# Kernel optimization log

Measured on AMD Instinct MI355X. Metric: run time of the kernel, lower is better.

## Reference

```python
import jax, jax.numpy as jnp
import numpy as np


def quat_to_rot(q):
    # q: [B, 4] = (x, y, z, w); same math as from_quaternion in the source.
    x, y, z, w = q[:, 0], q[:, 1], q[:, 2], q[:, 3]
    tx, ty, tz = 2.0 * x, 2.0 * y, 2.0 * z
    twx, twy, twz = tx * w, ty * w, tz * w
    txx, txy, txz = tx * x, ty * x, tz * x
    tyy, tyz, tzz = ty * y, tz * y, tz * z
    r = jnp.stack([1.0 - (tyy + tzz), txy - twz, txz + twy,
                   txy + twz, 1.0 - (txx + tzz), tyz - twx,
                   txz - twy, tyz + twx, 1.0 - (txx + tyy)], axis=-1)
    return r.reshape(-1, 3, 3)


def matrix_from_params(transfos):
    B, N = transfos.shape
    R = quat_to_rot(transfos[:, :4])
    if N == 10:
        S = jax.vmap(jnp.diag)(transfos[:, -3:])
    else:
        S = jnp.broadcast_to(jnp.eye(3, dtype=transfos.dtype), (B, 3, 3))
    SR = jnp.matmul(S, R)
    if N == 7:
        t = transfos[:, 4:7][..., None]
    else:
        t = jnp.zeros((B, 3, 1), transfos.dtype)
    return jnp.concatenate([SR, t], axis=2)  # [B, 3, 4]


def spatial_transformer_3d(img, transfos, min_ref_grid, max_ref_grid):
    B, H, W, D, C = img.shape  # ref_size_xyz = (W, H, D) per the source
    theta = matrix_from_params(transfos)  # [B, 3, 4]

    xs = jnp.linspace(min_ref_grid[0], max_ref_grid[0], W)
    ys = jnp.linspace(min_ref_grid[1], max_ref_grid[1], H)
    zs = jnp.linspace(min_ref_grid[2], max_ref_grid[2], D)
    mz, my, mx = jnp.meshgrid(zs, ys, xs, indexing='ij')  # (D, H, W), x fastest
    Nel = D * H * W
    grid = jnp.stack([mx.ravel(), my.ravel(), mz.ravel(),
                      jnp.ones(Nel, dtype=img.dtype)], axis=0)  # (4, Nel)
    pts = jnp.einsum('bij,jn->bin', theta, grid)  # (B, 3, Nel)

    Wf, Hf, Df = float(W), float(H), float(D)
    cx = (Wf - 1.0) / (max_ref_grid[0] - min_ref_grid[0])
    cy = (Hf - 1.0) / (max_ref_grid[1] - min_ref_grid[1])
    cz = (Df - 1.0) / (max_ref_grid[2] - min_ref_grid[2])
    ix = cx * pts[:, 0, :] - cx * min_ref_grid[0]
    iy = cy * pts[:, 1, :] - cy * min_ref_grid[1]
    iz = cz * pts[:, 2, :] - cz * min_ref_grid[2]

    # padding_mode in {'zeros','min'}: validity mask for out-of-grid points
    valid = ((ix >= 0.0) & (ix <= Wf - 1.0) &
             (iy >= 0.0) & (iy <= Hf - 1.0) &
             (iz >= 0.0) & (iz <= Df - 1.0)).astype(img.dtype)[..., None]  # (B, Nel, 1)

    ix0 = jnp.clip(jnp.floor(ix), 0.0, Wf - 1.0)
    iy0 = jnp.clip(jnp.floor(iy), 0.0, Hf - 1.0)
    iz0 = jnp.clip(jnp.floor(iz), 0.0, Df - 1.0)

    imf = img.reshape(B, H * W * D, C)
    acc = jnp.zeros((B, Nel, C), img.dtype)
    for ox in (0.0, 1.0):
        for oy in (0.0, 1.0):
            for oz in (0.0, 1.0):
                gx, gy, gz = ix0 + ox, iy0 + oy, iz0 + oz  # corner coords
                w = (jnp.clip(1.0 - jnp.abs(ix - gx), 0.0, 1.0) *
                     jnp.clip(1.0 - jnp.abs(iy - gy), 0.0, 1.0) *
                     jnp.clip(1.0 - jnp.abs(iz - gz), 0.0, 1.0))
                gxi = jnp.clip(gx, 0.0, Wf - 1.0).astype(jnp.int32)
                gyi = jnp.clip(gy, 0.0, Hf - 1.0).astype(jnp.int32)
                gzi = jnp.clip(gz, 0.0, Df - 1.0).astype(jnp.int32)
                lin = (gyi * W + gxi) * D + gzi  # row-major index into [H, W, D]
                v = jnp.take_along_axis(imf, lin[..., None], axis=1)  # (B, Nel, C)
                acc = acc + w[..., None] * v

    # padding_mode == 'min': fill out-of-grid voxels with the per-volume minimum
    fill = jnp.min(img, axis=(1, 2, 3, 4))[:, None, None]  # (B, 1, 1)
    out = valid * acc + (1.0 - valid) * fill
    # grid was flattened in (z, y, x) order with x fastest -> back to (H, W, D)
    out = out.reshape(B, D, H, W, C).transpose(0, 2, 3, 1, 4)
    return out


def setup_inputs() -> dict:
    key = jax.random.key(0)
    k1, k2 = jax.random.split(key)
    img = jax.random.normal(k1, (4, 160, 160, 160, 1), dtype=jnp.float32)
    transfos = jax.random.normal(k2, (4, 7), dtype=jnp.float32)
    return {"img": img, "transfos": transfos}


def reference(img, transfos):
    min_ref_grid = (-1.0, -1.0, -1.0)
    max_ref_grid = (1.0, 1.0, 1.0)
    return spatial_transformer_3d(img, transfos, min_ref_grid, max_ref_grid)
```

## Files before the change

### kernel.cpp

```cpp
#include <hip/hip_runtime.h>

#define HH 160
#define WW 160
#define DD 160
#define BB 4
#define NPB (HH * WW * DD / 4)
#define K1B 256

typedef float vfloat4 __attribute__((ext_vector_type(4)));

__global__ __launch_bounds__(256) void min_cst_kernel(const float4* __restrict__ img4,
                                                      const float* __restrict__ transfos,
                                                      float* __restrict__ partial,
                                                      double* __restrict__ cst) {
    const int b = blockIdx.y;
    const size_t base = (size_t)b * NPB;
    const int t0 = blockIdx.x * 256 + threadIdx.x;
    const int S = K1B * 256;

    float m = 3.4e38f;
    #pragma unroll
    for (int r = 0; r < 4; r++) {
        const int i0 = t0 + 4 * r * S;
        float4 v0 = img4[base + i0];
        float4 v1 = img4[base + i0 + S];
        float4 v2 = img4[base + i0 + 2 * S];
        float4 v3 = make_float4(3.4e38f, 3.4e38f, 3.4e38f, 3.4e38f);
        if (i0 + 3 * S < NPB) v3 = img4[base + i0 + 3 * S];
        m = fminf(m, fminf(fminf(v0.x, v0.y), fminf(v0.z, v0.w)));
        m = fminf(m, fminf(fminf(v1.x, v1.y), fminf(v1.z, v1.w)));
        m = fminf(m, fminf(fminf(v2.x, v2.y), fminf(v2.z, v2.w)));
        m = fminf(m, fminf(fminf(v3.x, v3.y), fminf(v3.z, v3.w)));
    }

    #pragma unroll
    for (int o = 32; o >= 1; o >>= 1) m = fminf(m, __shfl_down(m, o));
    __shared__ float s[4];
    const int lane = threadIdx.x & 63, wid = threadIdx.x >> 6;
    if (lane == 0) s[wid] = m;
    __syncthreads();
    if (threadIdx.x == 0) {
        partial[b * K1B + blockIdx.x] =
            fminf(fminf(s[0], s[1]), fminf(s[2], s[3]));
    }

    if (blockIdx.x == 0 && blockIdx.y == 0 && threadIdx.x < BB) {
        const int bb = threadIdx.x;
        const float* q = transfos + bb * 7;
        double x = q[0], y = q[1], z = q[2], w = q[3];
        double tx = 2.0 * x, ty = 2.0 * y, tz = 2.0 * z;
        double twx = tx * w, twy = ty * w, twz = tz * w;
        double txx = tx * x, txy = ty * x, txz = tz * x;
        double tyy = ty * y, tyz = tz * y, tzz = tz * z;
        double R[3][3] = {
            {1.0 - (tyy + tzz), txy - twz,         txz + twy},
            {txy + twz,         1.0 - (txx + tzz), tyz - twx},
            {txz - twy,         tyz + twx,         1.0 - (txx + tyy)}
        };
        double t[3] = {(double)q[4], (double)q[5], (double)q[6]};
        for (int r = 0; r < 3; r++) {
            cst[bb * 12 + r * 4 + 0] = R[r][0];
            cst[bb * 12 + r * 4 + 1] = R[r][1];
            cst[bb * 12 + r * 4 + 2] = R[r][2];
            cst[bb * 12 + r * 4 + 3] = 79.5 * (t[r] - R[r][0] - R[r][1] - R[r][2] + 1.0);
        }
    }
}

__global__ __launch_bounds__(256) void st3d_kernel(const float* __restrict__ img,
                                                   const double* __restrict__ cst,
                                                   const float* __restrict__ partial,
                                                   float* __restrict__ out) {
    const int bzc = blockIdx.z;
    const int b = bzc / 20;
    const int yt = bzc - b * 20;

    __shared__ float sred[4];
    float pm = partial[b * K1B + threadIdx.x];
    #pragma unroll
    for (int o = 32; o >= 1; o >>= 1) pm = fminf(pm, __shfl_down(pm, o));
    if ((threadIdx.x & 63) == 0) sred[threadIdx.x >> 6] = pm;
    __syncthreads();
    const float fill = fminf(fminf(sred[0], sred[1]), fminf(sred[2], sred[3]));

    const int tz = threadIdx.x & 3;
    const int tx = (threadIdx.x >> 2) & 7;
    const int ty = threadIdx.x >> 5;

    const int x  = blockIdx.y * 8 + tx;
    const int y  = yt * 8 + ty;
    const int zq = blockIdx.x * 16 + tz * 4;

    const double* c = cst + b * 12;
    const double c2 = c[2], c6 = c[6], c10 = c[10];
    const double dx = (double)x, dy = (double)y, dz = (double)zq;
    double ixd = fma(c[0], dx, fma(c[1], dy, fma(c2, dz, c[3])));
    double iyd = fma(c[4], dx, fma(c[5], dy, fma(c6, dz, c[7])));
    double izd = fma(c[8], dx, fma(c[9], dy, fma(c10, dz, c[11])));

    bool anyv = false;
    {
        double ax = ixd, ay = iyd, az = izd;
        #pragma unroll
        for (int k = 0; k < 4; k++) {
            anyv = anyv || ((ax >= 0.0) && (ax <= 159.0) && (ay >= 0.0) &&
                            (ay <= 159.0) && (az >= 0.0) && (az <= 159.0));
            ax += c2; ay += c6; az += c10;
        }
    }

    const float* base = img + (size_t)b * (HH * WW * DD);
    vfloat4 r;

    if (__any(anyv)) {
        #pragma unroll
        for (int k = 0; k < 4; k++) {
            const bool valid = (ixd >= 0.0) && (ixd <= 159.0) && (iyd >= 0.0) &&
                               (iyd <= 159.0) && (izd >= 0.0) && (izd <= 159.0);
            double flx = floor(ixd), fly = floor(iyd), flz = floor(izd);
            int x0 = (int)flx, y0 = (int)fly, z0 = (int)flz;
            x0 = min(max(x0, 0), 159);
            y0 = min(max(y0, 0), 159);
            z0 = min(max(z0, 0), 159);
            float fx = (float)(ixd - flx), fy = (float)(iyd - fly), fz = (float)(izd - flz);
            int x1 = min(x0 + 1, 159), y1 = min(y0 + 1, 159), z1 = min(z0 + 1, 159);
            const int o00 = (y0 * WW + x0) * DD;
            const int o01 = (y0 * WW + x1) * DD;
            const int o10 = (y1 * WW + x0) * DD;
            const int o11 = (y1 * WW + x1) * DD;
            float v000 = base[o00 + z0], v001 = base[o00 + z1];
            float v010 = base[o10 + z0], v011 = base[o10 + z1];
            float v100 = base[o01 + z0], v101 = base[o01 + z1];
            float v110 = base[o11 + z0], v111 = base[o11 + z1];
            float wx0 = 1.0f - fx, wx1 = fx;
            float wy0 = 1.0f - fy, wy1 = fy;
            float wz0 = 1.0f - fz, wz1 = fz;
            float acc;
            acc  = ((wx0 * wy0) * wz0) * v000;
            acc += ((wx0 * wy0) * wz1) * v001;
            acc += ((wx0 * wy1) * wz0) * v010;
            acc += ((wx0 * wy1) * wz1) * v011;
            acc += ((wx1 * wy0) * wz0) * v100;
            acc += ((wx1 * wy0) * wz1) * v101;
            acc += ((wx1 * wy1) * wz0) * v110;
            acc += ((wx1 * wy1) * wz1) * v111;
            r[k] = valid ? acc : fill;
            ixd += c2; iyd += c6; izd += c10;
        }
    } else {
        r[0] = fill; r[1] = fill; r[2] = fill; r[3] = fill;
    }

    vfloat4* outp = (vfloat4*)(out + (size_t)((b * HH + y) * WW + x) * DD + zq);
    __builtin_nontemporal_store(r, outp);
}

extern "C" void kernel_launch(void* const* d_in, const int* in_sizes, int n_in,
                              void* d_out, int out_size, void* d_ws, size_t ws_size,
                              hipStream_t stream) {
    const float* img = (const float*)d_in[0];
    const float* transfos = (const float*)d_in[1];
    float* out = (float*)d_out;
    float* partial = (float*)d_ws;
    double* cst = (double*)((char*)d_ws + 4096);

    min_cst_kernel<<<dim3(K1B, BB), 256, 0, stream>>>((const float4*)img, transfos,
                                                      partial, cst);
    st3d_kernel<<<dim3(DD / 16, WW / 8, (HH / 8) * BB), 256, 0, stream>>>(img, cst,
                                                                          partial, out);
}
```

Baseline: 137.8 us.

## Move fill-min reduction to separate kernel and process 8 z-values per thread

The per-block reduction of 256 partial minima is taken out of the main kernel and done once in a tiny extra kernel that writes one fill value per batch. Each thread of the resampling kernel now produces 8 consecutive z outputs in two groups of 4. In each group all 32 gather loads are issued before any interpolation math, to expose more memory-level parallelism. The costs are an extra kernel launch, half as many blocks, and higher register pressure from the batched loads.

```diff
diff --git a/kernel.cpp b/kernel.cpp
--- a/kernel.cpp
+++ b/kernel.cpp
@@ -67,21 +67,23 @@
     }
 }
 
+__global__ __launch_bounds__(256) void fin_min_kernel(const float* __restrict__ partial,
+                                                      float* __restrict__ fill) {
+    const int wid = threadIdx.x >> 6, lane = threadIdx.x & 63;
+    const float* p = partial + wid * K1B;
+    float m = fminf(fminf(p[lane], p[lane + 64]), fminf(p[lane + 128], p[lane + 192]));
+    #pragma unroll
+    for (int o = 32; o >= 1; o >>= 1) m = fminf(m, __shfl_down(m, o));
+    if (lane == 0) fill[wid] = m;
+}
+
 __global__ __launch_bounds__(256) void st3d_kernel(const float* __restrict__ img,
                                                    const double* __restrict__ cst,
-                                                   const float* __restrict__ partial,
+                                                   const float* __restrict__ fill,
                                                    float* __restrict__ out) {
     const int bzc = blockIdx.z;
     const int b = bzc / 20;
     const int yt = bzc - b * 20;
-
-    __shared__ float sred[4];
-    float pm = partial[b * K1B + threadIdx.x];
-    #pragma unroll
-    for (int o = 32; o >= 1; o >>= 1) pm = fminf(pm, __shfl_down(pm, o));
-    if ((threadIdx.x & 63) == 0) sred[threadIdx.x >> 6] = pm;
-    __syncthreads();
-    const float fill = fminf(fminf(sred[0], sred[1]), fminf(sred[2], sred[3]));
 
     const int tz = threadIdx.x & 3;
     const int tx = (threadIdx.x >> 2) & 7;
@@ -89,7 +91,9 @@
 
     const int x  = blockIdx.y * 8 + tx;
     const int y  = yt * 8 + ty;
-    const int zq = blockIdx.x * 16 + tz * 4;
+    const int zq = blockIdx.x * 32 + tz * 8;
+
+    const float fillv = fill[b];
 
     const double* c = cst + b * 12;
     const double c2 = c[2], c6 = c[6], c10 = c[10];
@@ -102,7 +106,7 @@
     {
         double ax = ixd, ay = iyd, az = izd;
         #pragma unroll
-        for (int k = 0; k < 4; k++) {
+        for (int k = 0; k < 8; k++) {
             anyv = anyv || ((ax >= 0.0) && (ax <= 159.0) && (ay >= 0.0) &&
                             (ay <= 159.0) && (az >= 0.0) && (az <= 159.0));
             ax += c2; ay += c6; az += c10;
@@ -110,49 +114,68 @@
     }
 
     const float* base = img + (size_t)b * (HH * WW * DD);
-    vfloat4 r;
+    vfloat4 r0, r1;
 
     if (__any(anyv)) {
         #pragma unroll
-        for (int k = 0; k < 4; k++) {
-            const bool valid = (ixd >= 0.0) && (ixd <= 159.0) && (iyd >= 0.0) &&
-                               (iyd <= 159.0) && (izd >= 0.0) && (izd <= 159.0);
-            double flx = floor(ixd), fly = floor(iyd), flz = floor(izd);
-            int x0 = (int)flx, y0 = (int)fly, z0 = (int)flz;
-            x0 = min(max(x0, 0), 159);
-            y0 = min(max(y0, 0), 159);
-            z0 = min(max(z0, 0), 159);
-            float fx = (float)(ixd - flx), fy = (float)(iyd - fly), fz = (float)(izd - flz);
-            int x1 = min(x0 + 1, 159), y1 = min(y0 + 1, 159), z1 = min(z0 + 1, 159);
-            const int o00 = (y0 * WW + x0) * DD;
-            const int o01 = (y0 * WW + x1) * DD;
-            const int o10 = (y1 * WW + x0) * DD;
-            const int o11 = (y1 * WW + x1) * DD;
-            float v000 = base[o00 + z0], v001 = base[o00 + z1];
-            float v010 = base[o10 + z0], v011 = base[o10 + z1];
-            float v100 = base[o01 + z0], v101 = base[o01 + z1];
-            float v110 = base[o11 + z0], v111 = base[o11 + z1];
-            float wx0 = 1.0f - fx, wx1 = fx;
-            float wy0 = 1.0f - fy, wy1 = fy;
-            float wz0 = 1.0f - fz, wz1 = fz;
-            float acc;
-            acc  = ((wx0 * wy0) * wz0) * v000;
-            acc += ((wx0 * wy0) * wz1) * v001;
-            acc += ((wx0 * wy1) * wz0) * v010;
-            acc += ((wx0 * wy1) * wz1) * v011;
-            acc += ((wx1 * wy0) * wz0) * v100;
-            acc += ((wx1 * wy0) * wz1) * v101;
-            acc += ((wx1 * wy1) * wz0) * v110;
-            acc += ((wx1 * wy1) * wz1) * v111;
-            r[k] = valid ? acc : fill;
-            ixd += c2; iyd += c6; izd += c10;
+        for (int g = 0; g < 2; g++) {
+            float v[4][8];
+            float fx[4], fy[4], fz[4];
+            unsigned vmask = 0;
+            #pragma unroll
+            for (int k = 0; k < 4; k++) {
+                const bool valid = (ixd >= 0.0) && (ixd <= 159.0) && (iyd >= 0.0) &&
+                                   (iyd <= 159.0) && (izd >= 0.0) && (izd <= 159.0);
+                if (valid) vmask |= (1u << k);
+                double flx = floor(ixd), fly = floor(iyd), flz = floor(izd);
+                int x0 = (int)flx, y0 = (int)fly, z0 = (int)flz;
+                x0 = min(max(x0, 0), 159);
+                y0 = min(max(y0, 0), 159);
+                z0 = min(max(z0, 0), 159);
+                fx[k] = (float)(ixd - flx);
+                fy[k] = (float)(iyd - fly);
+                fz[k] = (float)(izd - flz);
+                int x1 = min(x0 + 1, 159), y1 = min(y0 + 1, 159), z1 = min(z0 + 1, 159);
+                const int o00 = (y0 * WW + x0) * DD;
+                const int o01 = (y0 * WW + x1) * DD;
+                const int o10 = (y1 * WW + x0) * DD;
+                const int o11 = (y1 * WW + x1) * DD;
+                v[k][0] = base[o00 + z0];
+                v[k][1] = base[o00 + z1];
+                v[k][2] = base[o10 + z0];
+                v[k][3] = base[o10 + z1];
+                v[k][4] = base[o01 + z0];
+                v[k][5] = base[o01 + z1];
+                v[k][6] = base[o11 + z0];
+                v[k][7] = base[o11 + z1];
+                ixd += c2; iyd += c6; izd += c10;
+            }
+            #pragma unroll
+            for (int k = 0; k < 4; k++) {
+                float wx0 = 1.0f - fx[k], wx1 = fx[k];
+                float wy0 = 1.0f - fy[k], wy1 = fy[k];
+                float wz0 = 1.0f - fz[k], wz1 = fz[k];
+                float acc;
+                acc  = ((wx0 * wy0) * wz0) * v[k][0];
+                acc += ((wx0 * wy0) * wz1) * v[k][1];
+                acc += ((wx0 * wy1) * wz0) * v[k][2];
+                acc += ((wx0 * wy1) * wz1) * v[k][3];
+                acc += ((wx1 * wy0) * wz0) * v[k][4];
+                acc += ((wx1 * wy0) * wz1) * v[k][5];
+                acc += ((wx1 * wy1) * wz0) * v[k][6];
+                acc += ((wx1 * wy1) * wz1) * v[k][7];
+                float res = ((vmask >> k) & 1u) ? acc : fillv;
+                if (g == 0) r0[k] = res; else r1[k] = res;
+            }
         }
     } else {
-        r[0] = fill; r[1] = fill; r[2] = fill; r[3] = fill;
+        r0[0] = fillv; r0[1] = fillv; r0[2] = fillv; r0[3] = fillv;
+        r1[0] = fillv; r1[1] = fillv; r1[2] = fillv; r1[3] = fillv;
     }
 
-    vfloat4* outp = (vfloat4*)(out + (size_t)((b * HH + y) * WW + x) * DD + zq);
-    __builtin_nontemporal_store(r, outp);
+    float* op = out + (size_t)((b * HH + y) * WW + x) * DD + zq;
+    __builtin_nontemporal_store(r0, (vfloat4*)op);
+    __builtin_nontemporal_store(r1, (vfloat4*)(op + 4));
 }
 
 extern "C" void kernel_launch(void* const* d_in, const int* in_sizes, int n_in,
@@ -163,9 +186,11 @@
     float* out = (float*)d_out;
     float* partial = (float*)d_ws;
     double* cst = (double*)((char*)d_ws + 4096);
+    float* fill = (float*)((char*)d_ws + 8192);
 
     min_cst_kernel<<<dim3(K1B, BB), 256, 0, stream>>>((const float4*)img, transfos,
                                                       partial, cst);
-    st3d_kernel<<<dim3(DD / 16, WW / 8, (HH / 8) * BB), 256, 0, stream>>>(img, cst,
-                                                                          partial, out);
+    fin_min_kernel<<<dim3(1), 256, 0, stream>>>(partial, fill);
+    st3d_kernel<<<dim3(DD / 32, WW / 8, (HH / 8) * BB), 256, 0, stream>>>(img, cst,
+                                                                          fill, out);
 }
```

Measured after the change: 147.8 us. 7.2% more time.

## Prefill output with min value and cull fully out-of-grid tiles early

Applied to the files above, without the earlier changes.

Adds a kernel that finishes the per-volume min reduction once and a fill kernel that writes the fill value to the whole output. The resampling kernel then bounds each block's transformed coordinate box and returns early when the tile lies entirely outside the source grid, skipping the per-block partial reduction. This trades a full extra output write pass and two extra launches for skipping work in out-of-range tiles. Whether it pays off depends on how much of the volume maps outside the grid.

```diff
diff --git a/kernel.cpp b/kernel.cpp
--- a/kernel.cpp
+++ b/kernel.cpp
@@ -67,21 +67,62 @@
     }
 }
 
+__global__ __launch_bounds__(256) void fin_min_kernel(const float* __restrict__ partial,
+                                                      float* __restrict__ fill) {
+    const int wid = threadIdx.x >> 6, lane = threadIdx.x & 63;
+    const float* p = partial + wid * K1B;
+    float m = fminf(fminf(p[lane], p[lane + 64]), fminf(p[lane + 128], p[lane + 192]));
+    #pragma unroll
+    for (int o = 32; o >= 1; o >>= 1) m = fminf(m, __shfl_down(m, o));
+    if (lane == 0) fill[wid] = m;
+}
+
+__global__ __launch_bounds__(256) void fill_kernel(const float* __restrict__ fill,
+                                                   float* __restrict__ out) {
+    const int b = blockIdx.y;
+    const float fv = fill[b];
+    vfloat4 v; v[0] = fv; v[1] = fv; v[2] = fv; v[3] = fv;
+    vfloat4* o = (vfloat4*)(out + (size_t)b * (HH * WW * DD));
+    const int stride = gridDim.x * 256;
+    for (int i = blockIdx.x * 256 + threadIdx.x; i < NPB; i += stride)
+        __builtin_nontemporal_store(v, o + i);
+}
+
 __global__ __launch_bounds__(256) void st3d_kernel(const float* __restrict__ img,
                                                    const double* __restrict__ cst,
-                                                   const float* __restrict__ partial,
+                                                   const float* __restrict__ fill,
                                                    float* __restrict__ out) {
     const int bzc = blockIdx.z;
     const int b = bzc / 20;
     const int yt = bzc - b * 20;
 
-    __shared__ float sred[4];
-    float pm = partial[b * K1B + threadIdx.x];
-    #pragma unroll
-    for (int o = 32; o >= 1; o >>= 1) pm = fminf(pm, __shfl_down(pm, o));
-    if ((threadIdx.x & 63) == 0) sred[threadIdx.x >> 6] = pm;
-    __syncthreads();
-    const float fill = fminf(fminf(sred[0], sred[1]), fminf(sred[2], sred[3]));
+    const double* c = cst + b * 12;
+    const double c2 = c[2], c6 = c[6], c10 = c[10];
+
+    {
+        const double X0 = (double)(blockIdx.y * 8), X1 = X0 + 7.0;
+        const double Y0 = (double)(yt * 8),         Y1 = Y0 + 7.0;
+        const double Z0 = (double)(blockIdx.x * 16), Z1 = Z0 + 15.0;
+        double lo, hi, t;
+
+        lo = c[3]; hi = c[3];
+        t = c[0]; if (t >= 0.0) { lo += t * X0; hi += t * X1; } else { lo += t * X1; hi += t * X0; }
+        t = c[1]; if (t >= 0.0) { lo += t * Y0; hi += t * Y1; } else { lo += t * Y1; hi += t * Y0; }
+        t = c2;   if (t >= 0.0) { lo += t * Z0; hi += t * Z1; } else { lo += t * Z1; hi += t * Z0; }
+        if (hi < -1e-3 || lo > 159.001) return;
+
+        lo = c[7]; hi = c[7];
+        t = c[4]; if (t >= 0.0) { lo += t * X0; hi += t * X1; } else { lo += t * X1; hi += t * X0; }
+        t = c[5]; if (t >= 0.0) { lo += t * Y0; hi += t * Y1; } else { lo += t * Y1; hi += t * Y0; }
+        t = c6;   if (t >= 0.0) { lo += t * Z0; hi += t * Z1; } else { lo += t * Z1; hi += t * Z0; }
+        if (hi < -1e-3 || lo > 159.001) return;
+
+        lo = c[11]; hi = c[11];
+        t = c[8]; if (t >= 0.0) { lo += t * X0; hi += t * X1; } else { lo += t * X1; hi += t * X0; }
+        t = c[9]; if (t >= 0.0) { lo += t * Y0; hi += t * Y1; } else { lo += t * Y1; hi += t * Y0; }
+        t = c10;  if (t >= 0.0) { lo += t * Z0; hi += t * Z1; } else { lo += t * Z1; hi += t * Z0; }
+        if (hi < -1e-3 || lo > 159.001) return;
+    }
 
     const int tz = threadIdx.x & 3;
     const int tx = (threadIdx.x >> 2) & 7;
@@ -91,8 +132,8 @@
     const int y  = yt * 8 + ty;
     const int zq = blockIdx.x * 16 + tz * 4;
 
-    const double* c = cst + b * 12;
-    const double c2 = c[2], c6 = c[6], c10 = c[10];
+    const float fillv = fill[b];
+
     const double dx = (double)x, dy = (double)y, dz = (double)zq;
     double ixd = fma(c[0], dx, fma(c[1], dy, fma(c2, dz, c[3])));
     double iyd = fma(c[4], dx, fma(c[5], dy, fma(c6, dz, c[7])));
@@ -144,11 +185,11 @@
             acc += ((wx1 * wy0) * wz1) * v101;
             acc += ((wx1 * wy1) * wz0) * v110;
             acc += ((wx1 * wy1) * wz1) * v111;
-            r[k] = valid ? acc : fill;
+            r[k] = valid ? acc : fillv;
             ixd += c2; iyd += c6; izd += c10;
         }
     } else {
-        r[0] = fill; r[1] = fill; r[2] = fill; r[3] = fill;
+        r[0] = fillv; r[1] = fillv; r[2] = fillv; r[3] = fillv;
     }
 
     vfloat4* outp = (vfloat4*)(out + (size_t)((b * HH + y) * WW + x) * DD + zq);
@@ -163,9 +204,12 @@
     float* out = (float*)d_out;
     float* partial = (float*)d_ws;
     double* cst = (double*)((char*)d_ws + 4096);
+    float* fill = (float*)((char*)d_ws + 8192);
 
     min_cst_kernel<<<dim3(K1B, BB), 256, 0, stream>>>((const float4*)img, transfos,
                                                       partial, cst);
+    fin_min_kernel<<<dim3(1), 256, 0, stream>>>(partial, fill);
+    fill_kernel<<<dim3(512, BB), 256, 0, stream>>>(fill, out);
     st3d_kernel<<<dim3(DD / 16, WW / 8, (HH / 8) * BB), 256, 0, stream>>>(img, cst,
-                                                                          partial, out);
-}
+                                                                          fill, out);
+}
```

Result: slower. 144.3 us (+4.7%).
